# Optimization experiments

Measured on AMD Instinct MI355X. Metric: run time of the kernel, lower is better.

The kernel has to match this reference:

```python
import jax, jax.numpy as jnp
import numpy as np

WS = 8           # window size
NUM_HEADS = 16
DIM = 512
HEAD_DIM = DIM // NUM_HEADS


def _relative_position_index(ws):
    coords = np.stack(np.meshgrid(np.arange(ws), np.arange(ws), indexing='ij'))  # (2, ws, ws)
    cf = coords.reshape(2, -1)                                   # (2, ws*ws)
    rel = cf[:, :, None] - cf[:, None, :]                        # (2, N, N)
    rel = rel.transpose(1, 2, 0).copy()
    rel[:, :, 0] += ws - 1
    rel[:, :, 1] += ws - 1
    rel[:, :, 0] *= 2 * ws - 1
    return jnp.asarray(rel.sum(-1))                              # (N, N) int


REL_IDX = _relative_position_index(WS)


def setup_inputs() -> dict:
    key = jax.random.key(0)
    ks = jax.random.split(key, 4)
    B, C, H, W = 4, DIM, 128, 128
    x = jax.random.normal(ks[0], (B, C, H, W), dtype=jnp.float32)
    gamma = jnp.ones((DIM,), jnp.float32)
    beta = jnp.zeros((DIM,), jnp.float32)
    w_qkv = jax.random.normal(ks[1], (DIM, 3 * DIM), jnp.float32) * (DIM ** -0.5)
    w_proj = jax.random.normal(ks[2], (DIM, DIM), jnp.float32) * (DIM ** -0.5)
    b_proj = jnp.zeros((DIM,), jnp.float32)
    bias_table = jax.random.normal(ks[3], ((2 * WS - 1) ** 2, NUM_HEADS), jnp.float32) * 0.02
    return {"x": x, "gamma": gamma, "beta": beta, "w_qkv": w_qkv,
            "w_proj": w_proj, "b_proj": b_proj, "bias_table": bias_table}


def reference(x, gamma, beta, w_qkv, w_proj, b_proj, bias_table):
    B, C, H, W = x.shape
    pad_h = (WS - H % WS) % WS
    pad_w = (WS - W % WS) % WS
    x = jnp.pad(x, ((0, 0), (0, 0), (0, pad_h), (0, pad_w)))
    Hp, Wp = H + pad_h, W + pad_w
    nh, nw = Hp // WS, Wp // WS
    N = WS * WS  # tokens per window

    # window partition: (B,C,Hp,Wp) -> (B*nh*nw, N, C)
    xw = x.reshape(B, C, nh, WS, nw, WS).transpose(0, 2, 4, 3, 5, 1)
    xw = xw.reshape(B * nh * nw, N, C)

    # LayerNorm over channels
    mu = jnp.mean(xw, axis=-1, keepdims=True)
    var = jnp.var(xw, axis=-1, keepdims=True)
    xn = (xw - mu) * jax.lax.rsqrt(var + 1e-5) * gamma + beta

    # QKV projection (no bias)
    qkv = (xn @ w_qkv).reshape(-1, N, 3, NUM_HEADS, HEAD_DIM)
    qkv = qkv.transpose(2, 0, 3, 1, 4)   # (3, nWin, heads, N, hd)
    q, k, v = qkv[0], qkv[1], qkv[2]

    scale = HEAD_DIM ** -0.5
    attn = jnp.einsum('whnd,whmd->whnm', q, k) * scale          # (nWin, heads, N, N)
    rel_bias = bias_table[REL_IDX]                               # (N, N, heads)
    attn = attn + rel_bias.transpose(2, 0, 1)[None]
    attn = jax.nn.softmax(attn, axis=-1)

    out = jnp.einsum('whnm,whmd->wnhd', attn, v).reshape(-1, N, C)
    out = out @ w_proj + b_proj

    # un-window: (B*nh*nw, N, C) -> (B, C, Hp, Wp)
    out = out.reshape(B, nh, nw, WS, WS, C).transpose(0, 5, 1, 3, 2, 4)
    out = out.reshape(B, C, Hp, Wp)
    return out[:, :, :H, :W]
```

## Files before the change

### kernel.cpp

```cpp
#include <hip/hip_runtime.h>

typedef unsigned short u16;
typedef unsigned int u32;
typedef __bf16 bf16x8 __attribute__((ext_vector_type(8)));
typedef float f32x4 __attribute__((ext_vector_type(4)));

#define C_DIM 512
#define QKV_N 1536
#define KDIM 512
#define NHEAD 16
#define HD 32
#define H_IMG 128
#define W_IMG 128
#define HW 16384
#define NTOK 65536
#define NWIN 1024

#define GLL(g, l) __builtin_amdgcn_global_load_lds( \
    (const __attribute__((address_space(1))) u32*)(g), \
    (__attribute__((address_space(3))) u32*)(l), 16, 0, 0)

#define BAR() __builtin_amdgcn_s_barrier()
#define LGKM0() asm volatile("s_waitcnt lgkmcnt(0)" ::: "memory")
#define VM6() asm volatile("s_waitcnt vmcnt(6)" ::: "memory")
#define VM4() asm volatile("s_waitcnt vmcnt(4)" ::: "memory")
#define VM0() asm volatile("s_waitcnt vmcnt(0)" ::: "memory")

__device__ __forceinline__ u16 f2bf(float f) {
    u32 u = __builtin_bit_cast(u32, f);
    u += 0x7fffu + ((u >> 16) & 1u);
    return (u16)(u >> 16);
}

__global__ void sa_prep_kernel(const float* __restrict__ w_qkv,
                               const float* __restrict__ w_proj,
                               const float* __restrict__ bias_table,
                               u16* __restrict__ wqT, u16* __restrict__ wpT,
                               float* __restrict__ biasP) {
    int t = blockIdx.x * 256 + threadIdx.x;
    const int W1 = KDIM * QKV_N;
    const int W2 = KDIM * C_DIM;
    const int W3 = NHEAD * 64 * 64;
    if (t < W1) {
        int k = t / QKV_N, n = t % QKV_N;
        wqT[n * KDIM + k] = f2bf(w_qkv[t]);
    } else if (t < W1 + W2) {
        int u = t - W1;
        int k = u / C_DIM, n = u % C_DIM;
        wpT[n * KDIM + k] = f2bf(w_proj[u]);
    } else if (t < W1 + W2 + W3) {
        int u = t - W1 - W2;
        int h = u >> 12, n = (u >> 6) & 63, m = u & 63;
        int di = (n >> 3) - (m >> 3) + 7;
        int dj = (n & 7) - (m & 7) + 7;
        biasP[u] = bias_table[(di * 15 + dj) * NHEAD + h];
    }
}

__global__ __launch_bounds__(256) void sa_ln_stats_kernel(const float* __restrict__ x,
                                   float* __restrict__ mu, float* __restrict__ rsig) {
    __shared__ float ssum[4][64][4];
    __shared__ float ssq[4][64][4];
    int q  = threadIdx.x & 63;
    int cq = threadIdx.x >> 6;
    int quad = blockIdx.x * 64 + q;
    int tok4 = quad * 4;
    int b = tok4 >> 14, s = tok4 & (HW - 1);
    const float* xp = x + (size_t)b * C_DIM * HW + (size_t)cq * 128 * HW + s;
    float sx = 0.f, sy = 0.f, sz = 0.f, sw = 0.f;
    float qx = 0.f, qy = 0.f, qz = 0.f, qw = 0.f;
#pragma unroll 4
    for (int c = 0; c < 128; ++c) {
        float4 v = *reinterpret_cast<const float4*>(xp + (size_t)c * HW);
        sx += v.x; sy += v.y; sz += v.z; sw += v.w;
        qx += v.x * v.x; qy += v.y * v.y; qz += v.z * v.z; qw += v.w * v.w;
    }
    ssum[cq][q][0] = sx; ssum[cq][q][1] = sy; ssum[cq][q][2] = sz; ssum[cq][q][3] = sw;
    ssq[cq][q][0] = qx;  ssq[cq][q][1] = qy;  ssq[cq][q][2] = qz;  ssq[cq][q][3] = qw;
    __syncthreads();
    if (threadIdx.x < 64) {
#pragma unroll
        for (int j = 0; j < 4; ++j) {
            float S = ssum[0][q][j] + ssum[1][q][j] + ssum[2][q][j] + ssum[3][q][j];
            float Q = ssq[0][q][j] + ssq[1][q][j] + ssq[2][q][j] + ssq[3][q][j];
            float m = S * (1.f / C_DIM);
            float var = Q * (1.f / C_DIM) - m * m;
            mu[tok4 + j] = m;
            rsig[tok4 + j] = rsqrtf(var + 1e-5f);
        }
    }
}

__global__ __launch_bounds__(256) void sa_ln_norm_kernel(const float* __restrict__ x,
        const float* __restrict__ gamma, const float* __restrict__ beta,
        const float* __restrict__ mu, const float* __restrict__ rsig,
        u16* __restrict__ xnc) {
    __shared__ float tile[64][129];
    __shared__ float smu[64], srs[64];
    int b = blockIdx.x >> 10;
    int r = blockIdx.x & 1023;
    int win = r >> 2;
    int c0 = (r & 3) * 128;
    int wh = win >> 4, ww = win & 15;
    int tid = threadIdx.x;
    int n = tid & 63;
    int s_base = (wh * 8) * W_IMG + ww * 8;
    if (tid < 64) {
        int s = s_base + (tid >> 3) * W_IMG + (tid & 7);
        smu[tid] = mu[b * HW + s];
        srs[tid] = rsig[b * HW + s];
    }
    int s_n = s_base + (n >> 3) * W_IMG + (n & 7);
    const float* xb = x + (size_t)b * C_DIM * HW;
#pragma unroll
    for (int it = 0; it < 32; ++it) {
        int cl = it * 4 + (tid >> 6);
        tile[n][cl] = xb[(size_t)(c0 + cl) * HW + s_n];
    }
    __syncthreads();
    int cl = tid & 127;
    float g = gamma[c0 + cl], be = beta[c0 + cl];
#pragma unroll
    for (int it = 0; it < 32; ++it) {
        int nn = it * 2 + (tid >> 7);
        float v = (tile[nn][cl] - smu[nn]) * srs[nn] * g + be;
        xnc[(size_t)(((b << 8) + win) * 64 + nn) * C_DIM + c0 + cl] = f2bf(v);
    }
}


#define LDA1(Q,J,KK,BUF) af[Q][J][KK] = *reinterpret_cast<const bf16x8*>( \
    &lds[(BUF)*16384 + (wr*128 + ((Q)*2+(J))*16 + lr)*64 + ((((KK)*4)+lg) ^ ((lr&3)<<1))*8])
#define LDAQ(Q,BUF) do{ LDA1(Q,0,0,BUF); LDA1(Q,0,1,BUF); LDA1(Q,1,0,BUF); LDA1(Q,1,1,BUF); }while(0)
#define LDB1(NF,KK,BUF) bfr[NF][KK] = *reinterpret_cast<const bf16x8*>( \
    &lds[32768 + (BUF)*16384 + (wc*64 + (NF)*16 + lr)*64 + ((((KK)*4)+lg) ^ ((lr&3)<<1))*8])
#define LDB(BUF) do{ LDB1(0,0,BUF); LDB1(0,1,BUF); LDB1(1,0,BUF); LDB1(1,1,BUF); \
                     LDB1(2,0,BUF); LDB1(2,1,BUF); LDB1(3,0,BUF); LDB1(3,1,BUF); }while(0)
#define MFMA1(M,N,KK) acc[M][N] = __builtin_amdgcn_mfma_f32_16x16x32_bf16(af[(M)/2][(M)&1][KK], bfr[N][KK], acc[M][N], 0, 0, 0)
#define MFMAQ(Q) do{ __builtin_amdgcn_s_setprio(1); \
    MFMA1(2*(Q),0,0);   MFMA1(2*(Q),0,1);   MFMA1(2*(Q),1,0);   MFMA1(2*(Q),1,1); \
    MFMA1(2*(Q),2,0);   MFMA1(2*(Q),2,1);   MFMA1(2*(Q),3,0);   MFMA1(2*(Q),3,1); \
    MFMA1(2*(Q)+1,0,0); MFMA1(2*(Q)+1,0,1); MFMA1(2*(Q)+1,1,0); MFMA1(2*(Q)+1,1,1); \
    MFMA1(2*(Q)+1,2,0); MFMA1(2*(Q)+1,2,1); MFMA1(2*(Q)+1,3,0); MFMA1(2*(Q)+1,3,1); \
    __builtin_amdgcn_s_setprio(0); }while(0)
#define STAGE_A(KT, H) do{ const u16* _s = Asrc + (KT)*64 + (size_t)((H)*128)*KDIM; \
    u16* _d = Adst + ((KT)&1)*16384 + (H)*8192; \
    GLL(_s, _d); GLL(_s + (size_t)64*KDIM, _d + 4096); }while(0)
#define STAGE_B(KT, H) do{ const u16* _s = Bsrc + (KT)*64 + (size_t)((H)*128)*KDIM; \
    u16* _d = Bdst + ((KT)&1)*16384 + (H)*8192; \
    GLL(_s, _d); GLL(_s + (size_t)64*KDIM, _d + 4096); }while(0)

template <int EPI>
__global__ __launch_bounds__(512, 2) void sa_gemm8_kernel(const u16* __restrict__ A,
        const u16* __restrict__ BT, u16* __restrict__ outB, float* __restrict__ outF,
        const float* __restrict__ bias, int nbx, int NT) {
    __shared__ u16 lds[65536];

    const int tid = threadIdx.x;
    const int cpx = gridDim.x >> 3;
    const int wg = (blockIdx.x & 7) * cpx + (blockIdx.x >> 3);
    const int mb = wg / nbx, nb = wg % nbx;
    const int m0 = mb * 256, n0 = nb * 256;
    const int lane = tid & 63, wv = tid >> 6;
    const int wr = wv >> 2, wc = wv & 3;
    const int lr = lane & 15, lg = lane >> 4;

    const int arow = tid >> 3;
    const int axs = ((tid & 7) ^ ((arow & 3) << 1)) * 8;
    const u16* Asrc = A  + (size_t)(m0 + arow) * KDIM + axs;
    const u16* Bsrc = BT + (size_t)(n0 + arow) * KDIM + axs;
    u16* Adst = lds + tid * 8;
    u16* Bdst = lds + 32768 + tid * 8;

    f32x4 acc[8][4];
#pragma unroll
    for (int i = 0; i < 8; ++i)
#pragma unroll
        for (int j = 0; j < 4; ++j) acc[i][j] = {0.f, 0.f, 0.f, 0.f};
    bf16x8 af[4][2][2];
    bf16x8 bfr[4][2];

    STAGE_A(0, 0); STAGE_A(0, 1); STAGE_B(0, 0); STAGE_B(0, 1);
    VM4();
    STAGE_A(1, 0); STAGE_B(1, 0); STAGE_B(1, 1);
    VM6();
    BAR();

#pragma unroll 1
    for (int i = 0; i < 3; ++i) {
        LDB(0); LDAQ(0, 0); STAGE_A(2*i + 1, 1);
        BAR(); LGKM0(); MFMAQ(0); BAR();
        LDAQ(1, 0); LDAQ(2, 0); STAGE_B(2*i + 2, 0);
        BAR(); LGKM0(); MFMAQ(1); BAR();
        LDAQ(3, 0); STAGE_B(2*i + 2, 1);
        BAR(); LGKM0(); MFMAQ(2); BAR();
        STAGE_A(2*i + 2, 0);
        BAR(); LGKM0(); MFMAQ(3); VM6(); BAR();
        LDB(1); LDAQ(0, 1); STAGE_A(2*i + 2, 1);
        BAR(); LGKM0(); MFMAQ(0); BAR();
        LDAQ(1, 1); LDAQ(2, 1); STAGE_B(2*i + 3, 0);
        BAR(); LGKM0(); MFMAQ(1); BAR();
        LDAQ(3, 1); STAGE_B(2*i + 3, 1);
        BAR(); LGKM0(); MFMAQ(2); BAR();
        STAGE_A(2*i + 3, 0);
        BAR(); LGKM0(); MFMAQ(3); VM6(); BAR();
    }
    LDB(0); LDAQ(0, 0); STAGE_A(7, 1);
    BAR(); LGKM0(); MFMAQ(0); BAR();
    LDAQ(1, 0); LDAQ(2, 0);
    BAR(); LGKM0(); MFMAQ(1); BAR();
    LDAQ(3, 0);
    BAR(); LGKM0(); MFMAQ(2); BAR();
    BAR(); LGKM0(); MFMAQ(3); VM0(); BAR();
    LDB(1); LDAQ(0, 1);
    BAR(); LGKM0(); MFMAQ(0); BAR();
    LDAQ(1, 1); LDAQ(2, 1);
    BAR(); LGKM0(); MFMAQ(1); BAR();
    LDAQ(3, 1);
    BAR(); LGKM0(); MFMAQ(2); BAR();
    BAR(); LGKM0(); MFMAQ(3);

    if (EPI == 0) {
#pragma unroll
        for (int mf = 0; mf < 8; ++mf) {
#pragma unroll
            for (int nf = 0; nf < 4; ++nf) {
                int col = n0 + wc * 64 + nf * 16 + lr;
                int row = m0 + wr * 128 + mf * 16 + lg * 4;
#pragma unroll
                for (int rr = 0; rr < 4; ++rr)
                    outB[(size_t)(row + rr) * NT + col] = f2bf(acc[mf][nf][rr]);
            }
        }
    } else {
        int win0 = m0 >> 6;
        int b_img = win0 >> 8, wl = win0 & 255;
        int h0 = (wl >> 4) * 8, w0 = (wl & 15) * 8;
        float* fbuf = reinterpret_cast<float*>(lds);
        __syncthreads();
#pragma unroll
        for (int s = 0; s < 2; ++s) {
            if ((wc >> 1) == s) {
                int half = wc & 1;
                float* cb = fbuf + half * 16384;
#pragma unroll
                for (int mf = 0; mf < 8; ++mf) {
#pragma unroll
                    for (int nf = 0; nf < 4; ++nf) {
                        int cp = nf * 16 + lr;
                        int row = wr * 128 + mf * 16 + lg * 4;
                        int h = (row >> 3) & 7;
                        int sl = ((row >> 6) & 3) * 2 + ((row >> 2) & 1);
                        float bb = bias[n0 + (2 * s + half) * 64 + cp];
                        f32x4 v = acc[mf][nf];
                        float4 o = {v[0] + bb, v[1] + bb, v[2] + bb, v[3] + bb};
                        *reinterpret_cast<float4*>(&cb[cp * 256 + h * 32 + (sl ^ (cp & 7)) * 4]) = o;
                    }
                }
            }
            __syncthreads();
#pragma unroll
            for (int j = 0; j < 16; ++j) {
                int flat = j * 512 + tid;
                int half = flat >> 12, f = flat & 4095;
                int cp = f >> 6, h = (f >> 3) & 7, sl = f & 7;
                int col = n0 + (2 * s + half) * 64 + cp;
                float4 v = *reinterpret_cast<const float4*>(
                    &fbuf[half * 16384 + cp * 256 + h * 32 + ((sl ^ (cp & 7))) * 4]);
                *reinterpret_cast<float4*>(outF + (size_t)(b_img * C_DIM + col) * HW
                                           + (size_t)(h0 + h) * W_IMG + w0 + sl * 4) = v;
            }
            __syncthreads();
        }
    }
}

__global__ __launch_bounds__(64) void sa_attn_kernel(const u16* __restrict__ qkv,
        const float* __restrict__ biasP, u16* __restrict__ attnc) {
    __shared__ u16 VT[32 * 80];
    __shared__ u16 Ps[64 * 80];
    int win = blockIdx.x >> 4, head = blockIdx.x & 15;
    int lane = threadIdx.x, lr = lane & 15, lg = lane >> 4;
    const u16* base = qkv + (size_t)win * 64 * QKV_N + head * HD;

#pragma unroll
    for (int p = 0; p < 4; ++p) {
        int idx = p * 64 + lane;
        int row = idx >> 2, seg = idx & 3;
        union { uint4 u; u16 s[8]; } cv;
        cv.u = *reinterpret_cast<const uint4*>(base + (size_t)row * QKV_N + 1024 + seg * 8);
#pragma unroll
        for (int e = 0; e < 8; ++e) VT[(seg * 8 + e) * 80 + row] = cv.s[e];
    }

    bf16x8 qa[4], kb[4];
#pragma unroll
    for (int mt = 0; mt < 4; ++mt)
        qa[mt] = *reinterpret_cast<const bf16x8*>(base + (size_t)(mt * 16 + lr) * QKV_N + lg * 8);
#pragma unroll
    for (int nt = 0; nt < 4; ++nt)
        kb[nt] = *reinterpret_cast<const bf16x8*>(base + (size_t)(nt * 16 + lr) * QKV_N + 512 + lg * 8);

    f32x4 sacc[4][4];
#pragma unroll
    for (int i = 0; i < 4; ++i)
#pragma unroll
        for (int j = 0; j < 4; ++j) sacc[i][j] = {0.f, 0.f, 0.f, 0.f};
#pragma unroll
    for (int mt = 0; mt < 4; ++mt)
#pragma unroll
        for (int nt = 0; nt < 4; ++nt)
            sacc[mt][nt] = __builtin_amdgcn_mfma_f32_16x16x32_bf16(qa[mt], kb[nt], sacc[mt][nt], 0, 0, 0);

    __syncthreads();

    const float scale = 0.17677669529663687f;
    const float* bp = biasP + head * 64 * 64;
#pragma unroll
    for (int mt = 0; mt < 4; ++mt) {
#pragma unroll
        for (int rr = 0; rr < 4; ++rr) {
            int row = mt * 16 + lg * 4 + rr;
            float vals[4];
#pragma unroll
            for (int nt = 0; nt < 4; ++nt)
                vals[nt] = sacc[mt][nt][rr] * scale + bp[row * 64 + nt * 16 + lr];
            float mx = fmaxf(fmaxf(vals[0], vals[1]), fmaxf(vals[2], vals[3]));
#pragma unroll
            for (int d = 1; d < 16; d <<= 1) mx = fmaxf(mx, __shfl_xor(mx, d, 64));
            float sm = 0.f;
#pragma unroll
            for (int nt = 0; nt < 4; ++nt) { vals[nt] = __expf(vals[nt] - mx); sm += vals[nt]; }
#pragma unroll
            for (int d = 1; d < 16; d <<= 1) sm += __shfl_xor(sm, d, 64);
            float inv = 1.f / sm;
#pragma unroll
            for (int nt = 0; nt < 4; ++nt)
                Ps[row * 80 + nt * 16 + lr] = f2bf(vals[nt] * inv);
        }
    }
    __syncthreads();

    f32x4 oacc[4][2];
#pragma unroll
    for (int i = 0; i < 4; ++i) { oacc[i][0] = {0.f,0.f,0.f,0.f}; oacc[i][1] = {0.f,0.f,0.f,0.f}; }
#pragma unroll
    for (int ks = 0; ks < 2; ++ks) {
        bf16x8 pa[4], vb[2];
#pragma unroll
        for (int mt = 0; mt < 4; ++mt)
            pa[mt] = *reinterpret_cast<const bf16x8*>(&Ps[(mt * 16 + lr) * 80 + ks * 32 + lg * 8]);
#pragma unroll
        for (int n2 = 0; n2 < 2; ++n2)
            vb[n2] = *reinterpret_cast<const bf16x8*>(&VT[(n2 * 16 + lr) * 80 + ks * 32 + lg * 8]);
#pragma unroll
        for (int mt = 0; mt < 4; ++mt)
#pragma unroll
            for (int n2 = 0; n2 < 2; ++n2)
                oacc[mt][n2] = __builtin_amdgcn_mfma_f32_16x16x32_bf16(pa[mt], vb[n2], oacc[mt][n2], 0, 0, 0);
    }

#pragma unroll
    for (int mt = 0; mt < 4; ++mt)
#pragma unroll
        for (int n2 = 0; n2 < 2; ++n2)
#pragma unroll
            for (int rr = 0; rr < 4; ++rr) {
                int row = mt * 16 + lg * 4 + rr;
                attnc[(size_t)(win * 64 + row) * C_DIM + head * HD + n2 * 16 + lr] =
                    f2bf(oacc[mt][n2][rr]);
            }
}

extern "C" void kernel_launch(void* const* d_in, const int* in_sizes, int n_in,
                              void* d_out, int out_size, void* d_ws, size_t ws_size,
                              hipStream_t stream) {
    const float* x          = (const float*)d_in[0];
    const float* gamma      = (const float*)d_in[1];
    const float* beta       = (const float*)d_in[2];
    const float* w_qkv      = (const float*)d_in[3];
    const float* w_proj     = (const float*)d_in[4];
    const float* b_proj     = (const float*)d_in[5];
    const float* bias_table = (const float*)d_in[6];
    float* out = (float*)d_out;

    char* ws = (char*)d_ws;
    size_t off = 0;
    auto alloc = [&](size_t bytes) {
        char* p = ws + off;
        off += (bytes + 255) & ~(size_t)255;
        return p;
    };
    u16*   wqT   = (u16*)alloc((size_t)KDIM * QKV_N * 2);
    u16*   wpT   = (u16*)alloc((size_t)KDIM * C_DIM * 2);
    float* biasP = (float*)alloc((size_t)NHEAD * 64 * 64 * 4);
    float* mu    = (float*)alloc((size_t)NTOK * 4);
    float* rsig  = (float*)alloc((size_t)NTOK * 4);
    u16*   xnc   = (u16*)alloc((size_t)NTOK * C_DIM * 2);
    u16*   qkvc  = (u16*)alloc((size_t)NTOK * QKV_N * 2);
    u16*   attnc = (u16*)alloc((size_t)NTOK * C_DIM * 2);

    sa_prep_kernel<<<4352, 256, 0, stream>>>(w_qkv, w_proj, bias_table, wqT, wpT, biasP);
    sa_ln_stats_kernel<<<256, 256, 0, stream>>>(x, mu, rsig);
    sa_ln_norm_kernel<<<4096, 256, 0, stream>>>(x, gamma, beta, mu, rsig, xnc);
    sa_gemm8_kernel<0><<<256 * 6, 512, 0, stream>>>(xnc, wqT, qkvc, nullptr, nullptr, 6, QKV_N);
    sa_attn_kernel<<<NWIN * NHEAD, 64, 0, stream>>>(qkvc, biasP, attnc);
    sa_gemm8_kernel<1><<<256 * 2, 512, 0, stream>>>(attnc, wpT, nullptr, out, b_proj, 2, C_DIM);
}
```

Baseline: 377.8 us.

## Fuse LayerNorm stats and normalize into one per-window kernel; widen LDS swizzle

Merges the separate LayerNorm statistics pass and normalize pass into one kernel where each block loads a full 64-token by 512-channel window into LDS, computes mean and variance there, and writes bf16 output. This removes a second full read of the fp32 input and the mu/rsig round trip through global memory. The block uses about 130KB of LDS, which limits occupancy to one block per CU, and the bf16 stores are now 2-byte scalar writes. Separately, the GEMM LDS XOR swizzle changes from (row&3)<<1 to row&7 to cut bank conflicts on the A/B fragment loads.

```diff
diff --git a/kernel.cpp b/kernel.cpp
--- a/kernel.cpp
+++ b/kernel.cpp
@@ -57,83 +57,62 @@
     }
 }
 
-__global__ __launch_bounds__(256) void sa_ln_stats_kernel(const float* __restrict__ x,
-                                   float* __restrict__ mu, float* __restrict__ rsig) {
-    __shared__ float ssum[4][64][4];
-    __shared__ float ssq[4][64][4];
-    int q  = threadIdx.x & 63;
-    int cq = threadIdx.x >> 6;
-    int quad = blockIdx.x * 64 + q;
-    int tok4 = quad * 4;
-    int b = tok4 >> 14, s = tok4 & (HW - 1);
-    const float* xp = x + (size_t)b * C_DIM * HW + (size_t)cq * 128 * HW + s;
-    float sx = 0.f, sy = 0.f, sz = 0.f, sw = 0.f;
-    float qx = 0.f, qy = 0.f, qz = 0.f, qw = 0.f;
-#pragma unroll 4
-    for (int c = 0; c < 128; ++c) {
-        float4 v = *reinterpret_cast<const float4*>(xp + (size_t)c * HW);
-        sx += v.x; sy += v.y; sz += v.z; sw += v.w;
-        qx += v.x * v.x; qy += v.y * v.y; qz += v.z * v.z; qw += v.w * v.w;
-    }
-    ssum[cq][q][0] = sx; ssum[cq][q][1] = sy; ssum[cq][q][2] = sz; ssum[cq][q][3] = sw;
-    ssq[cq][q][0] = qx;  ssq[cq][q][1] = qy;  ssq[cq][q][2] = qz;  ssq[cq][q][3] = qw;
-    __syncthreads();
-    if (threadIdx.x < 64) {
-#pragma unroll
-        for (int j = 0; j < 4; ++j) {
-            float S = ssum[0][q][j] + ssum[1][q][j] + ssum[2][q][j] + ssum[3][q][j];
-            float Q = ssq[0][q][j] + ssq[1][q][j] + ssq[2][q][j] + ssq[3][q][j];
-            float m = S * (1.f / C_DIM);
-            float var = Q * (1.f / C_DIM) - m * m;
-            mu[tok4 + j] = m;
-            rsig[tok4 + j] = rsqrtf(var + 1e-5f);
-        }
-    }
-}
-
-__global__ __launch_bounds__(256) void sa_ln_norm_kernel(const float* __restrict__ x,
+__global__ __launch_bounds__(512) void sa_ln_fused_kernel(const float* __restrict__ x,
         const float* __restrict__ gamma, const float* __restrict__ beta,
-        const float* __restrict__ mu, const float* __restrict__ rsig,
         u16* __restrict__ xnc) {
-    __shared__ float tile[64][129];
+    __shared__ float tile[64 * 513];
+    __shared__ float ssum[8][64], ssq[8][64];
     __shared__ float smu[64], srs[64];
-    int b = blockIdx.x >> 10;
-    int r = blockIdx.x & 1023;
-    int win = r >> 2;
-    int c0 = (r & 3) * 128;
-    int wh = win >> 4, ww = win & 15;
+    int win = blockIdx.x;
+    int b = win >> 8, wl = win & 255;
+    int wh = wl >> 4, ww = wl & 15;
     int tid = threadIdx.x;
     int n = tid & 63;
-    int s_base = (wh * 8) * W_IMG + ww * 8;
+    int g = tid >> 6;
+    int s_n = (wh * 8 + (n >> 3)) * W_IMG + ww * 8 + (n & 7);
+    const float* xb = x + (size_t)b * C_DIM * HW + s_n;
+    float sum = 0.f, sq = 0.f;
+#pragma unroll 8
+    for (int it = 0; it < 64; ++it) {
+        int c = it * 8 + g;
+        float v = xb[(size_t)c * HW];
+        tile[n * 513 + c] = v;
+        sum += v; sq += v * v;
+    }
+    ssum[g][n] = sum; ssq[g][n] = sq;
+    __syncthreads();
     if (tid < 64) {
-        int s = s_base + (tid >> 3) * W_IMG + (tid & 7);
-        smu[tid] = mu[b * HW + s];
-        srs[tid] = rsig[b * HW + s];
-    }
-    int s_n = s_base + (n >> 3) * W_IMG + (n & 7);
-    const float* xb = x + (size_t)b * C_DIM * HW;
-#pragma unroll
-    for (int it = 0; it < 32; ++it) {
-        int cl = it * 4 + (tid >> 6);
-        tile[n][cl] = xb[(size_t)(c0 + cl) * HW + s_n];
+        float S = 0.f, Q = 0.f;
+#pragma unroll
+        for (int k = 0; k < 8; ++k) { S += ssum[k][n]; Q += ssq[k][n]; }
+        float m = S * (1.f / C_DIM);
+        float var = Q * (1.f / C_DIM) - m * m;
+        smu[n] = m; srs[n] = rsqrtf(var + 1e-5f);
     }
     __syncthreads();
-    int cl = tid & 127;
-    float g = gamma[c0 + cl], be = beta[c0 + cl];
-#pragma unroll
-    for (int it = 0; it < 32; ++it) {
-        int nn = it * 2 + (tid >> 7);
-        float v = (tile[nn][cl] - smu[nn]) * srs[nn] * g + be;
-        xnc[(size_t)(((b << 8) + win) * 64 + nn) * C_DIM + c0 + cl] = f2bf(v);
+    float gg[8], bb[8];
+#pragma unroll
+    for (int c0 = 0; c0 < 8; ++c0) { gg[c0] = gamma[c0 * 64 + n]; bb[c0] = beta[c0 * 64 + n]; }
+#pragma unroll
+    for (int it = 0; it < 8; ++it) {
+        int nn = it * 8 + g;
+        float m = smu[nn], r = srs[nn];
+        u16* op = xnc + (size_t)((win << 6) + nn) * C_DIM;
+#pragma unroll
+        for (int c0 = 0; c0 < 8; ++c0) {
+            int c = c0 * 64 + n;
+            float v = (tile[nn * 513 + c] - m) * r * gg[c0] + bb[c0];
+            op[c] = f2bf(v);
+        }
     }
 }
 
 
 #define LDA1(Q,J,KK,BUF) af[Q][J][KK] = *reinterpret_cast<const bf16x8*>( \
-    &lds[(BUF)*16384 + (wr*128 + ((Q)*2+(J))*16 + lr)*64 + ((((KK)*4)+lg) ^ ((lr&3)<<1))*8])
+    &lds[(BUF)*16384 + (wr*128 + ((Q)*2+(J))*16 + lr)*64 + ((((KK)*4)+lg) ^ (lr & 7))*8])
 #define LDAQ(Q,BUF) do{ LDA1(Q,0,0,BUF); LDA1(Q,0,1,BUF); LDA1(Q,1,0,BUF); LDA1(Q,1,1,BUF); }while(0)
 #define LDB1(NF,KK,BUF) bfr[NF][KK] = *reinterpret_cast<const bf16x8*>( \
-    &lds[32768 + (BUF)*16384 + (wc*64 + (NF)*16 + lr)*64 + ((((KK)*4)+lg) ^ ((lr&3)<<1))*8])
+    &lds[32768 + (BUF)*16384 + (wc*64 + (NF)*16 + lr)*64 + ((((KK)*4)+lg) ^ (lr & 7))*8])
 #define LDB(BUF) do{ LDB1(0,0,BUF); LDB1(0,1,BUF); LDB1(1,0,BUF); LDB1(1,1,BUF); \
                      LDB1(2,0,BUF); LDB1(2,1,BUF); LDB1(3,0,BUF); LDB1(3,1,BUF); }while(0)
 #define MFMA1(M,N,KK) acc[M][N] = __builtin_amdgcn_mfma_f32_16x16x32_bf16(af[(M)/2][(M)&1][KK], bfr[N][KK], acc[M][N], 0, 0, 0)
@@ -166,7 +145,7 @@
     const int lr = lane & 15, lg = lane >> 4;
 
     const int arow = tid >> 3;
-    const int axs = ((tid & 7) ^ ((arow & 3) << 1)) * 8;
+    const int axs = ((tid & 7) ^ ((tid >> 3) & 7)) * 8;
     const u16* Asrc = A  + (size_t)(m0 + arow) * KDIM + axs;
     const u16* Bsrc = BT + (size_t)(n0 + arow) * KDIM + axs;
     u16* Adst = lds + tid * 8;
@@ -251,9 +230,9 @@
                         int row = wr * 128 + mf * 16 + lg * 4;
                         int h = (row >> 3) & 7;
                         int sl = ((row >> 6) & 3) * 2 + ((row >> 2) & 1);
-                        float bb = bias[n0 + (2 * s + half) * 64 + cp];
+                        float bbv = bias[n0 + (2 * s + half) * 64 + cp];
                         f32x4 v = acc[mf][nf];
-                        float4 o = {v[0] + bb, v[1] + bb, v[2] + bb, v[3] + bb};
+                        float4 o = {v[0] + bbv, v[1] + bbv, v[2] + bbv, v[3] + bbv};
                         *reinterpret_cast<float4*>(&cb[cp * 256 + h * 32 + (sl ^ (cp & 7)) * 4]) = o;
                     }
                 }
@@ -394,15 +373,12 @@
     u16*   wqT   = (u16*)alloc((size_t)KDIM * QKV_N * 2);
     u16*   wpT   = (u16*)alloc((size_t)KDIM * C_DIM * 2);
     float* biasP = (float*)alloc((size_t)NHEAD * 64 * 64 * 4);
-    float* mu    = (float*)alloc((size_t)NTOK * 4);
-    float* rsig  = (float*)alloc((size_t)NTOK * 4);
     u16*   xnc   = (u16*)alloc((size_t)NTOK * C_DIM * 2);
     u16*   qkvc  = (u16*)alloc((size_t)NTOK * QKV_N * 2);
     u16*   attnc = (u16*)alloc((size_t)NTOK * C_DIM * 2);
 
     sa_prep_kernel<<<4352, 256, 0, stream>>>(w_qkv, w_proj, bias_table, wqT, wpT, biasP);
-    sa_ln_stats_kernel<<<256, 256, 0, stream>>>(x, mu, rsig);
-    sa_ln_norm_kernel<<<4096, 256, 0, stream>>>(x, gamma, beta, mu, rsig, xnc);
+    sa_ln_fused_kernel<<<NWIN, 512, 0, stream>>>(x, gamma, beta, xnc);
     sa_gemm8_kernel<0><<<256 * 6, 512, 0, stream>>>(xnc, wqT, qkvc, nullptr, nullptr, 6, QKV_N);
     sa_attn_kernel<<<NWIN * NHEAD, 64, 0, stream>>>(qkvc, biasP, attnc);
     sa_gemm8_kernel<1><<<256 * 2, 512, 0, stream>>>(attnc, wpT, nullptr, out, b_proj, 2, C_DIM);
```

New measurement: 381.6 us. Within noise of the previous version (+1.0%).
